# Performance work log

Hardware: AMD Instinct MI355X
Metric: run time of the kernel (lower is better)

The kernel has to match this reference:

```python
import jax, jax.numpy as jnp
import numpy as np

# Complete binary tree: B trees, L leaves each, processed level-synchronously.
B, L, IN_DIM, MEM = 64, 1024, 300, 256


def setup_inputs() -> dict:
    key = jax.random.key(0)
    ks = jax.random.split(key, 6)
    s = 0.05
    embs = jax.random.normal(ks[0], (B, L, IN_DIM), dtype=jnp.float32)
    # Leaf module: c = cx(x); h = sigmoid(ox(x)) * tanh(c)
    Wcx = jax.random.normal(ks[1], (MEM, IN_DIM), dtype=jnp.float32) * s
    bcx = jnp.zeros((MEM,), jnp.float32)
    Wox = jax.random.normal(ks[2], (MEM, IN_DIM), dtype=jnp.float32) * s
    box = jnp.zeros((MEM,), jnp.float32)
    # Composer: 4 gates (i, lf, rf, u), each gate = Linear(lh) + Linear(rh).
    # Stacked: Wl/Wr have shape [4, MEM, MEM]; biases [4, MEM].
    Wl = jax.random.normal(ks[3], (4, MEM, MEM), dtype=jnp.float32) * s
    bl = jnp.zeros((4, MEM), jnp.float32)
    Wr = jax.random.normal(ks[4], (4, MEM, MEM), dtype=jnp.float32) * s
    br = jnp.zeros((4, MEM), jnp.float32)
    return dict(embs=embs, Wcx=Wcx, bcx=bcx, Wox=Wox, box=box,
                Wl=Wl, bl=bl, Wr=Wr, br=br)


def reference(embs, Wcx, bcx, Wox, box, Wl, bl, Wr, br):
    # Leaf module (BinaryTreeLeafModule.forward), vectorized over all leaves.
    c = jnp.einsum('blx,mx->blm', embs, Wcx) + bcx          # [B, L, MEM]
    o = jax.nn.sigmoid(jnp.einsum('blx,mx->blm', embs, Wox) + box)
    h = o * jnp.tanh(c)

    bias = bl + br                                          # [4, MEM]
    n = c.shape[1]
    while n > 1:  # log2(L) levels, static unrolled loop
        lc, rc = c[:, 0::2], c[:, 1::2]                     # [B, n/2, MEM]
        lh, rh = h[:, 0::2], h[:, 1::2]
        # All 4 gate pre-activations fused: [B, n/2, 4, MEM]
        g = (jnp.einsum('bnm,gom->bngo', lh, Wl)
             + jnp.einsum('bnm,gom->bngo', rh, Wr) + bias)
        i = jax.nn.sigmoid(g[..., 0, :])
        lf = jax.nn.sigmoid(g[..., 1, :])
        rf = jax.nn.sigmoid(g[..., 2, :])
        u = jnp.tanh(g[..., 3, :])
        c = i * u + lf * lc + rf * rc                       # composer cell
        h = jnp.tanh(c)                                     # gate_output=False path
        n //= 2

    # Root state (tree.state = (c, h)); stacked as [2, B, MEM]
    return jnp.stack([c[:, 0], h[:, 0]])
```

## Files before the change

kernel.cpp:

```cpp
#include <hip/hip_runtime.h>
#include <hip/hip_bf16.h>


typedef __attribute__((ext_vector_type(8))) short bf16x8;
typedef __attribute__((ext_vector_type(4))) float f32x4;

__device__ __forceinline__ float fsig(float x)  { return 1.f / (1.f + __expf(-x)); }
__device__ __forceinline__ float ftanh(float x) { return 1.f - 2.f / (__expf(2.f * x) + 1.f); }
__device__ __forceinline__ ushort f2bf(float x) {
    __hip_bfloat16 b = __float2bfloat16(x);
    return *reinterpret_cast<ushort*>(&b);
}

__device__ __forceinline__ void gld_lds16(const void* g, void* l) {
    __builtin_amdgcn_global_load_lds((const __attribute__((address_space(1))) void*)g,
                                     (__attribute__((address_space(3))) void*)l, 16, 0, 0);
}

__global__ void prep(const float* __restrict__ Wl,  const float* __restrict__ Wr,
                     const float* __restrict__ bl,  const float* __restrict__ br,
                     const float* __restrict__ Wcx, const float* __restrict__ Wox,
                     const float* __restrict__ bcx, const float* __restrict__ box,
                     const float* __restrict__ embs,
                     ushort* __restrict__ Wb2, ushort* __restrict__ WbL,
                     float* __restrict__ bp2, float* __restrict__ bpL,
                     ushort* __restrict__ embsB)
{
    const int gid = blockIdx.x * 256 + threadIdx.x;
    for (int i = gid; i < 524288; i += 262144) {
        int e = i & 7, slot = (i >> 3) & 3, o = (i >> 5) & 255;
        int g = (i >> 13) & 3, t = i >> 15;
        int q = slot ^ ((o >> 1) & 3);
        int k = t * 32 + q * 8 + e;
        float v = (k < 256) ? Wl[(g * 256 + o) * 256 + k]
                            : Wr[(g * 256 + o) * 256 + (k - 256)];
        Wb2[i] = f2bf(v);
    }
    if (gid < 163840) {
        int e = gid & 7, slot = (gid >> 3) & 3, o = (gid >> 5) & 255;
        int g = (gid >> 13) & 1, t = gid >> 14;
        int q = slot ^ ((o >> 1) & 3);
        int k = t * 32 + q * 8 + e;
        float v = 0.f;
        if (k < 300) v = g ? Wox[o * 300 + k] : Wcx[o * 300 + k];
        WbL[gid] = f2bf(v);
    }
    if (gid < 1024) bp2[gid] = bl[gid] + br[gid];
    if (gid < 512) {
        int g = gid >> 8, o = gid & 255;
        bpL[gid] = g ? box[o] : bcx[o];
    }
    for (int i = gid; i < 65536 * 80; i += 262144) {
        int row = i / 80;
        int k = (i - row * 80) * 4;
        float4 v = make_float4(0.f, 0.f, 0.f, 0.f);
        if (k < 300) v = *(const float4*)(embs + (size_t)row * 300 + k);
        ushort4 o4;
        o4.x = f2bf(v.x); o4.y = f2bf(v.y); o4.z = f2bf(v.z); o4.w = f2bf(v.w);
        *(ushort4*)(embsB + (size_t)row * 320 + k) = o4;
    }
}

template<int NG, int HALVES, int MODE>
__global__ __launch_bounds__(256, 4)
void mfma_gemm(const ushort* __restrict__ A,
               const ushort* __restrict__ Wb,
               const float* __restrict__ bp,
               const float* __restrict__ Cprev,
               float* __restrict__ c_out,
               ushort* __restrict__ h_out,
               int M)
{
    constexpr int K = HALVES * 32;
    constexpr int OW = 128 / NG;
    __shared__ __align__(16) ushort As[2][512 * 8];
    __shared__ __align__(16) ushort Bs[2][512 * 8];

    const int tid = threadIdx.x;
    const int wid = tid >> 6, ln = tid & 63;
    const int lq = ln >> 4, lr = ln & 15;
    const int wm = wid >> 1, wn = wid & 1;
    const int rowBlk = blockIdx.x * 128;
    const int o0 = blockIdx.y * OW;

    f32x4 acc[4][4];
#pragma unroll
    for (int m = 0; m < 4; ++m)
#pragma unroll
        for (int f = 0; f < 4; ++f) acc[m][f] = f32x4{0.f, 0.f, 0.f, 0.f};

    const int ar0 = tid >> 2,  as0 = tid & 3;
    const int ar1 = ar0 + 64;
    const int aq0 = (as0 - ((ar0 >> 1) & 3)) & 3;
    const int aq1 = (as0 - ((ar1 >> 1) & 3)) & 3;
    const ushort* aP0 = A + (size_t)min(rowBlk + ar0, M - 1) * K + aq0 * 8;
    const ushort* aP1 = A + (size_t)min(rowBlk + ar1, M - 1) * K + aq1 * 8;
    const int bj0 = tid >> 2,        bs0 = tid & 3;
    const int bj1 = (tid + 256) >> 2;
    const int bg0 = bj0 / OW, bo0 = o0 + (bj0 & (OW - 1));
    const int bg1 = bj1 / OW, bo1 = o0 + (bj1 & (OW - 1));
    const ushort* bP0 = Wb + ((size_t)bg0 * 1024 + bo0 * 4 + bs0) * 8;
    const ushort* bP1 = Wb + ((size_t)bg1 * 1024 + bo1 * 4 + bs0) * 8;
    constexpr size_t BSTR = (size_t)NG * 1024 * 8;

    const int aSw = (lq + ((lr >> 1) & 3)) & 3;
    const int bSw = lq ^ ((lr >> 1) & 3);
    int aOff[4];
#pragma unroll
    for (int m = 0; m < 4; ++m)
        aOff[m] = ((wm * 64 + m * 16 + lr) * 4 + aSw) * 8;
    int bOff[4];
#pragma unroll
    for (int f = 0; f < 4; ++f)
        bOff[f] = ((f * 32 + wn * 16 + lr) * 4 + bSw) * 8;

    gld_lds16(aP0, &As[0][tid * 8]);
    gld_lds16(aP1, &As[0][(tid + 256) * 8]);
    gld_lds16(bP0, &Bs[0][tid * 8]);
    gld_lds16(bP1, &Bs[0][(tid + 256) * 8]);

#pragma unroll
    for (int h = 0; h < HALVES; ++h) {
        __syncthreads();
        const int cur = h & 1;
        if (h + 1 < HALVES) {
            gld_lds16(aP0 + (size_t)(h + 1) * 32, &As[cur ^ 1][tid * 8]);
            gld_lds16(aP1 + (size_t)(h + 1) * 32, &As[cur ^ 1][(tid + 256) * 8]);
            gld_lds16(bP0 + (size_t)(h + 1) * BSTR, &Bs[cur ^ 1][tid * 8]);
            gld_lds16(bP1 + (size_t)(h + 1) * BSTR, &Bs[cur ^ 1][(tid + 256) * 8]);
        }
        bf16x8 a[4];
#pragma unroll
        for (int m = 0; m < 4; ++m)
            a[m] = *(const bf16x8*)&As[cur][aOff[m]];
#pragma unroll
        for (int f = 0; f < 4; ++f) {
            bf16x8 b = *(const bf16x8*)&Bs[cur][bOff[f]];
#pragma unroll
            for (int m = 0; m < 4; ++m)
                acc[m][f] = __builtin_amdgcn_mfma_f32_16x16x32_bf16(a[m], b, acc[m][f], 0, 0, 0);
        }
    }

#pragma unroll
    for (int m = 0; m < 4; ++m) {
        const int row0 = rowBlk + wm * 64 + m * 16 + lq * 4;
        if constexpr (MODE == 0) {
#pragma unroll
            for (int ob = 0; ob < 2; ++ob) {
                const int col = o0 + ob * 32 + wn * 16 + lr;
                const float bc = bp[col], bo = bp[256 + col];
#pragma unroll
                for (int j = 0; j < 4; ++j) {
                    int row = row0 + j;
                    if (row < M) {
                        float cv = acc[m][ob][j] + bc;
                        float ov = acc[m][2 + ob][j] + bo;
                        c_out[(size_t)row * 256 + col] = cv;
                        h_out[(size_t)row * 256 + col] = f2bf(fsig(ov) * ftanh(cv));
                    }
                }
            }
        } else {
            const int col = o0 + wn * 16 + lr;
            const float bi  = bp[col],       blf = bp[256 + col];
            const float brf = bp[512 + col], bu  = bp[768 + col];
#pragma unroll
            for (int j = 0; j < 4; ++j) {
                int row = row0 + j;
                if (row < M) {
                    float gi = fsig(acc[m][0][j] + bi);
                    float lf = fsig(acc[m][1][j] + blf);
                    float rf = fsig(acc[m][2][j] + brf);
                    float gu = ftanh(acc[m][3][j] + bu);
                    float lc = Cprev[(size_t)row * 512 + col];
                    float rc = Cprev[(size_t)row * 512 + 256 + col];
                    float cv = gi * gu + lf * lc + rf * rc;
                    c_out[(size_t)row * 256 + col] = cv;
                    h_out[(size_t)row * 256 + col] = f2bf(ftanh(cv));
                }
            }
        }
    }
}


__global__ __launch_bounds__(512, 1)
void tail_lstm(const ushort* __restrict__ hin,
               const float* __restrict__ cin,
               const ushort* __restrict__ Wb,
               const float* __restrict__ bp,
               float* __restrict__ dout)
{
    __shared__ __align__(16) ushort H0[32 * 256];
    __shared__ __align__(16) ushort H1[16 * 256];
    __shared__ __align__(16) float  C0[32 * 256];
    __shared__ __align__(16) float  C1[16 * 256];

    const int b = blockIdx.x;
    const int tid = threadIdx.x;
    const int wid = tid >> 6, ln = tid & 63;
    const int lq = ln >> 4, lr = ln & 15;

    for (int ct = tid; ct < 1024; ct += 512) {
        int pr = ct >> 5, pc = ct & 31;
        bf16x8 v = *(const bf16x8*)(hin + ((size_t)(b * 32 + pr) * 256 + pc * 8));
        *(bf16x8*)&H0[pr * 256 + ((pc ^ ((pr >> 1) & 7)) * 8)] = v;
    }
    for (int i = tid; i < 2048; i += 512)
        *(float4*)&C0[i * 4] = *(const float4*)(cin + (size_t)b * 32 * 256 + i * 4);
    __syncthreads();

    int o_[2], sl_[2];
    const ushort* bB[2];
#pragma unroll
    for (int of = 0; of < 2; ++of) {
        o_[of] = wid * 32 + of * 16 + lr;
        sl_[of] = lq ^ ((o_[of] >> 1) & 3);
        bB[of] = Wb + (size_t)(o_[of] * 4 + sl_[of]) * 8;
    }
    const float bi  = bp[o_[0]],       blf = bp[256 + o_[0]];
    const float brf = bp[512 + o_[0]], bu  = bp[768 + o_[0]];
    const float bi1  = bp[o_[1]],       blf1 = bp[256 + o_[1]];
    const float brf1 = bp[512 + o_[1]], bu1  = bp[768 + o_[1]];

#pragma unroll 1
    for (int lvl = 0; lvl < 5; ++lvl) {
        const int npo = 16 >> lvl;
        const ushort* Hin = (lvl & 1) ? H1 : H0;
        ushort*       Hout = (lvl & 1) ? H0 : H1;
        const float*  Cin = (lvl & 1) ? C1 : C0;
        float*        Cout = (lvl & 1) ? C0 : C1;

        f32x4 acc[2][4];
#pragma unroll
        for (int of = 0; of < 2; ++of)
#pragma unroll
            for (int g = 0; g < 4; ++g) acc[of][g] = f32x4{0.f, 0.f, 0.f, 0.f};

        bf16x8 b0[2][4], b1[2][4], a0, a1;
#pragma unroll
        for (int of = 0; of < 2; ++of)
#pragma unroll
            for (int g = 0; g < 4; ++g)
                b0[of][g] = *(const bf16x8*)(bB[of] + (size_t)g * 8192);
        {
            int pr = 2 * lr, pc = lq;
            a0 = *(const bf16x8*)&Hin[pr * 256 + ((pc ^ ((pr >> 1) & 7)) * 8)];
        }

#pragma unroll 1
        for (int ks = 0; ks < 16; ks += 2) {
            if (ks + 1 < 16) {
#pragma unroll
                for (int of = 0; of < 2; ++of)
#pragma unroll
                    for (int g = 0; g < 4; ++g)
                        b1[of][g] = *(const bf16x8*)(bB[of] + (size_t)((ks + 1) * 4 + g) * 8192);
                int pr = 2 * lr + ((ks + 1) >> 3), pc = lq + ((ks + 1) & 7) * 4;
                a1 = *(const bf16x8*)&Hin[pr * 256 + ((pc ^ ((pr >> 1) & 7)) * 8)];
            }
#pragma unroll
            for (int of = 0; of < 2; ++of)
#pragma unroll
                for (int g = 0; g < 4; ++g)
                    acc[of][g] = __builtin_amdgcn_mfma_f32_16x16x32_bf16(a0, b0[of][g], acc[of][g], 0, 0, 0);
            if (ks + 2 < 16) {
#pragma unroll
                for (int of = 0; of < 2; ++of)
#pragma unroll
                    for (int g = 0; g < 4; ++g)
                        b0[of][g] = *(const bf16x8*)(bB[of] + (size_t)((ks + 2) * 4 + g) * 8192);
                int pr = 2 * lr + ((ks + 2) >> 3), pc = lq + ((ks + 2) & 7) * 4;
                a0 = *(const bf16x8*)&Hin[pr * 256 + ((pc ^ ((pr >> 1) & 7)) * 8)];
            }
#pragma unroll
            for (int of = 0; of < 2; ++of)
#pragma unroll
                for (int g = 0; g < 4; ++g)
                    acc[of][g] = __builtin_amdgcn_mfma_f32_16x16x32_bf16(a1, b1[of][g], acc[of][g], 0, 0, 0);
        }

#pragma unroll
        for (int of = 0; of < 2; ++of) {
            const int col = o_[of];
            const float vbi  = of ? bi1 : bi,   vblf = of ? blf1 : blf;
            const float vbrf = of ? brf1 : brf, vbu  = of ? bu1 : bu;
#pragma unroll
            for (int j = 0; j < 4; ++j) {
                int row = lq * 4 + j;
                if (row < npo) {
                    float gi = fsig(acc[of][0][j] + vbi);
                    float lf = fsig(acc[of][1][j] + vblf);
                    float rf = fsig(acc[of][2][j] + vbrf);
                    float gu = ftanh(acc[of][3][j] + vbu);
                    float lc = Cin[(2 * row) * 256 + col];
                    float rc = Cin[(2 * row + 1) * 256 + col];
                    float cv = gi * gu + lf * lc + rf * rc;
                    float hv = ftanh(cv);
                    if (lvl == 4) {
                        dout[b * 256 + col] = cv;
                        dout[16384 + b * 256 + col] = hv;
                    } else {
                        Cout[row * 256 + col] = cv;
                        Hout[row * 256 + (((col >> 3) ^ ((row >> 1) & 7)) * 8) + (col & 7)] = f2bf(hv);
                    }
                }
            }
        }
        __syncthreads();
    }
}


extern "C" void kernel_launch(void* const* d_in, const int* in_sizes, int n_in,
                              void* d_out, int out_size, void* d_ws, size_t ws_size,
                              hipStream_t stream)
{
    const float* embs = (const float*)d_in[0];
    const float* Wcx  = (const float*)d_in[1];
    const float* bcx  = (const float*)d_in[2];
    const float* Wox  = (const float*)d_in[3];
    const float* box  = (const float*)d_in[4];
    const float* Wl   = (const float*)d_in[5];
    const float* bl   = (const float*)d_in[6];
    const float* Wr   = (const float*)d_in[7];
    const float* br   = (const float*)d_in[8];

    char* p = (char*)d_ws;
    ushort* Wb2 = (ushort*)p;  p += (size_t)524288 * 2;
    ushort* WbL = (ushort*)p;  p += (size_t)163840 * 2;
    float*  bp2 = (float*)p;   p += 1024 * 4;
    float*  bpL = (float*)p;   p += 512 * 4;
    float*  c0  = (float*)p;   p += (size_t)65536 * 256 * 4;
    ushort* h0  = (ushort*)p;  p += (size_t)65536 * 256 * 2;
    char* X = p;
    ushort* embsB = (ushort*)X;
    float*  cA = (float*)X;
    ushort* hA = (ushort*)(X + (size_t)32768 * 256 * 4);
    float*  cB = (float*)(X + (size_t)48 * 1024 * 1024);
    ushort* hB = (ushort*)(X + (size_t)64 * 1024 * 1024);

    prep<<<1024, 256, 0, stream>>>(Wl, Wr, bl, br, Wcx, Wox, bcx, box, embs,
                                   Wb2, WbL, bp2, bpL, embsB);

    mfma_gemm<2, 10, 0><<<dim3(512, 4), 256, 0, stream>>>(
        embsB, WbL, bpL, nullptr, c0, h0, 65536);

    mfma_gemm<4, 16, 1><<<dim3(256, 8), 256, 0, stream>>>(
        h0, Wb2, bp2, c0, cA, hA, 32768);
    mfma_gemm<4, 16, 1><<<dim3(128, 8), 256, 0, stream>>>(
        hA, Wb2, bp2, cA, cB, hB, 16384);
    mfma_gemm<4, 16, 1><<<dim3(64, 8), 256, 0, stream>>>(
        hB, Wb2, bp2, cB, cA, hA, 8192);
    mfma_gemm<4, 16, 1><<<dim3(32, 8), 256, 0, stream>>>(
        hA, Wb2, bp2, cA, cB, hB, 4096);
    mfma_gemm<4, 16, 1><<<dim3(16, 8), 256, 0, stream>>>(
        hB, Wb2, bp2, cB, cA, hA, 2048);

    tail_lstm<<<64, 512, 0, stream>>>(
        hA, cA, Wb2, bp2, (float*)d_out);
}
```

Baseline: 260.3 us.

## Triple-buffer GEMM LDS loads and fold one more level into tail kernel

The GEMM moves from a double-buffered to a triple-buffered LDS pipeline, prefetching two K-slices ahead with explicit vmcnt waits and a raw barrier, and lowers the launch-bounds occupancy hint from 4 to 3. The tail kernel now starts one level earlier (64 nodes per tree) and handles that level with a two-row-tile MFMA pass, which removes the last small GEMM launch. This trades LDS footprint and occupancy for deeper load latency hiding, and replaces a poorly occupied launch with extra serial work inside 64 blocks.

```diff
diff --git a/kernel.cpp b/kernel.cpp
--- a/kernel.cpp
+++ b/kernel.cpp
@@ -61,8 +61,9 @@
     }
 }
 
+
 template<int NG, int HALVES, int MODE>
-__global__ __launch_bounds__(256, 4)
+__global__ __launch_bounds__(256, 3)
 void mfma_gemm(const ushort* __restrict__ A,
                const ushort* __restrict__ Wb,
                const float* __restrict__ bp,
@@ -73,8 +74,8 @@
 {
     constexpr int K = HALVES * 32;
     constexpr int OW = 128 / NG;
-    __shared__ __align__(16) ushort As[2][512 * 8];
-    __shared__ __align__(16) ushort Bs[2][512 * 8];
+    __shared__ __align__(16) ushort As[3][512 * 8];
+    __shared__ __align__(16) ushort Bs[3][512 * 8];
 
     const int tid = threadIdx.x;
     const int wid = tid >> 6, ln = tid & 63;
@@ -118,27 +119,42 @@
     gld_lds16(aP1, &As[0][(tid + 256) * 8]);
     gld_lds16(bP0, &Bs[0][tid * 8]);
     gld_lds16(bP1, &Bs[0][(tid + 256) * 8]);
+    gld_lds16(aP0 + 32, &As[1][tid * 8]);
+    gld_lds16(aP1 + 32, &As[1][(tid + 256) * 8]);
+    gld_lds16(bP0 + BSTR, &Bs[1][tid * 8]);
+    gld_lds16(bP1 + BSTR, &Bs[1][(tid + 256) * 8]);
+    asm volatile("s_waitcnt vmcnt(4)" ::: "memory");
+    __builtin_amdgcn_s_barrier();
+    __builtin_amdgcn_sched_barrier(0);
 
 #pragma unroll
     for (int h = 0; h < HALVES; ++h) {
-        __syncthreads();
-        const int cur = h & 1;
-        if (h + 1 < HALVES) {
-            gld_lds16(aP0 + (size_t)(h + 1) * 32, &As[cur ^ 1][tid * 8]);
-            gld_lds16(aP1 + (size_t)(h + 1) * 32, &As[cur ^ 1][(tid + 256) * 8]);
-            gld_lds16(bP0 + (size_t)(h + 1) * BSTR, &Bs[cur ^ 1][tid * 8]);
-            gld_lds16(bP1 + (size_t)(h + 1) * BSTR, &Bs[cur ^ 1][(tid + 256) * 8]);
+        const ushort* Ac = &As[h % 3][0];
+        const ushort* Bc = &Bs[h % 3][0];
+        if (h + 2 < HALVES) {
+            ushort* An = &As[(h + 2) % 3][0];
+            ushort* Bn = &Bs[(h + 2) % 3][0];
+            gld_lds16(aP0 + (size_t)(h + 2) * 32, An + tid * 8);
+            gld_lds16(aP1 + (size_t)(h + 2) * 32, An + (tid + 256) * 8);
+            gld_lds16(bP0 + (size_t)(h + 2) * BSTR, Bn + tid * 8);
+            gld_lds16(bP1 + (size_t)(h + 2) * BSTR, Bn + (tid + 256) * 8);
         }
         bf16x8 a[4];
 #pragma unroll
         for (int m = 0; m < 4; ++m)
-            a[m] = *(const bf16x8*)&As[cur][aOff[m]];
+            a[m] = *(const bf16x8*)(Ac + aOff[m]);
 #pragma unroll
         for (int f = 0; f < 4; ++f) {
-            bf16x8 b = *(const bf16x8*)&Bs[cur][bOff[f]];
+            bf16x8 b = *(const bf16x8*)(Bc + bOff[f]);
 #pragma unroll
             for (int m = 0; m < 4; ++m)
                 acc[m][f] = __builtin_amdgcn_mfma_f32_16x16x32_bf16(a[m], b, acc[m][f], 0, 0, 0);
+        }
+        if (h + 1 < HALVES) {
+            if (h + 2 < HALVES) asm volatile("s_waitcnt vmcnt(4)" ::: "memory");
+            else                asm volatile("s_waitcnt vmcnt(0)" ::: "memory");
+            __builtin_amdgcn_s_barrier();
+            __builtin_amdgcn_sched_barrier(0);
         }
     }
 
@@ -192,23 +208,23 @@
                const float* __restrict__ bp,
                float* __restrict__ dout)
 {
-    __shared__ __align__(16) ushort H0[32 * 256];
-    __shared__ __align__(16) ushort H1[16 * 256];
-    __shared__ __align__(16) float  C0[32 * 256];
-    __shared__ __align__(16) float  C1[16 * 256];
+    __shared__ __align__(16) ushort H0[64 * 256];
+    __shared__ __align__(16) ushort H1[32 * 256];
+    __shared__ __align__(16) float  C0[64 * 256];
+    __shared__ __align__(16) float  C1[32 * 256];
 
     const int b = blockIdx.x;
     const int tid = threadIdx.x;
     const int wid = tid >> 6, ln = tid & 63;
     const int lq = ln >> 4, lr = ln & 15;
 
-    for (int ct = tid; ct < 1024; ct += 512) {
+    for (int ct = tid; ct < 2048; ct += 512) {
         int pr = ct >> 5, pc = ct & 31;
-        bf16x8 v = *(const bf16x8*)(hin + ((size_t)(b * 32 + pr) * 256 + pc * 8));
+        bf16x8 v = *(const bf16x8*)(hin + ((size_t)(b * 64 + pr) * 256 + pc * 8));
         *(bf16x8*)&H0[pr * 256 + ((pc ^ ((pr >> 1) & 7)) * 8)] = v;
     }
-    for (int i = tid; i < 2048; i += 512)
-        *(float4*)&C0[i * 4] = *(const float4*)(cin + (size_t)b * 32 * 256 + i * 4);
+    for (int i = tid; i < 4096; i += 512)
+        *(float4*)&C0[i * 4] = *(const float4*)(cin + (size_t)b * 64 * 256 + i * 4);
     __syncthreads();
 
     int o_[2], sl_[2];
@@ -219,14 +235,102 @@
         sl_[of] = lq ^ ((o_[of] >> 1) & 3);
         bB[of] = Wb + (size_t)(o_[of] * 4 + sl_[of]) * 8;
     }
-    const float bi  = bp[o_[0]],       blf = bp[256 + o_[0]];
-    const float brf = bp[512 + o_[0]], bu  = bp[768 + o_[0]];
+    const float bi0  = bp[o_[0]],       blf0 = bp[256 + o_[0]];
+    const float brf0 = bp[512 + o_[0]], bu0  = bp[768 + o_[0]];
     const float bi1  = bp[o_[1]],       blf1 = bp[256 + o_[1]];
     const float brf1 = bp[512 + o_[1]], bu1  = bp[768 + o_[1]];
 
+    {
+        f32x4 acc[2][2][4];
+#pragma unroll
+        for (int m = 0; m < 2; ++m)
+#pragma unroll
+            for (int of = 0; of < 2; ++of)
+#pragma unroll
+                for (int g = 0; g < 4; ++g) acc[m][of][g] = f32x4{0.f, 0.f, 0.f, 0.f};
+
+        bf16x8 b0[2][4], b1[2][4], a0[2], a1[2];
+#pragma unroll
+        for (int of = 0; of < 2; ++of)
+#pragma unroll
+            for (int g = 0; g < 4; ++g)
+                b0[of][g] = *(const bf16x8*)(bB[of] + (size_t)g * 8192);
+#pragma unroll
+        for (int m = 0; m < 2; ++m) {
+            int pr = 32 * m + 2 * lr, pc = lq;
+            a0[m] = *(const bf16x8*)&H0[pr * 256 + ((pc ^ ((pr >> 1) & 7)) * 8)];
+        }
+
 #pragma unroll 1
-    for (int lvl = 0; lvl < 5; ++lvl) {
-        const int npo = 16 >> lvl;
+        for (int ks = 0; ks < 16; ks += 2) {
+            if (ks + 1 < 16) {
+#pragma unroll
+                for (int of = 0; of < 2; ++of)
+#pragma unroll
+                    for (int g = 0; g < 4; ++g)
+                        b1[of][g] = *(const bf16x8*)(bB[of] + (size_t)((ks + 1) * 4 + g) * 8192);
+#pragma unroll
+                for (int m = 0; m < 2; ++m) {
+                    int pr = 32 * m + 2 * lr + ((ks + 1) >> 3), pc = lq + ((ks + 1) & 7) * 4;
+                    a1[m] = *(const bf16x8*)&H0[pr * 256 + ((pc ^ ((pr >> 1) & 7)) * 8)];
+                }
+            }
+#pragma unroll
+            for (int m = 0; m < 2; ++m)
+#pragma unroll
+                for (int of = 0; of < 2; ++of)
+#pragma unroll
+                    for (int g = 0; g < 4; ++g)
+                        acc[m][of][g] = __builtin_amdgcn_mfma_f32_16x16x32_bf16(a0[m], b0[of][g], acc[m][of][g], 0, 0, 0);
+            if (ks + 2 < 16) {
+#pragma unroll
+                for (int of = 0; of < 2; ++of)
+#pragma unroll
+                    for (int g = 0; g < 4; ++g)
+                        b0[of][g] = *(const bf16x8*)(bB[of] + (size_t)((ks + 2) * 4 + g) * 8192);
+#pragma unroll
+                for (int m = 0; m < 2; ++m) {
+                    int pr = 32 * m + 2 * lr + ((ks + 2) >> 3), pc = lq + ((ks + 2) & 7) * 4;
+                    a0[m] = *(const bf16x8*)&H0[pr * 256 + ((pc ^ ((pr >> 1) & 7)) * 8)];
+                }
+            }
+#pragma unroll
+            for (int m = 0; m < 2; ++m)
+#pragma unroll
+                for (int of = 0; of < 2; ++of)
+#pragma unroll
+                    for (int g = 0; g < 4; ++g)
+                        acc[m][of][g] = __builtin_amdgcn_mfma_f32_16x16x32_bf16(a1[m], b1[of][g], acc[m][of][g], 0, 0, 0);
+        }
+
+#pragma unroll
+        for (int m = 0; m < 2; ++m)
+#pragma unroll
+        for (int of = 0; of < 2; ++of) {
+            const int col = o_[of];
+            const float vbi  = of ? bi1 : bi0,   vblf = of ? blf1 : blf0;
+            const float vbrf = of ? brf1 : brf0, vbu  = of ? bu1 : bu0;
+#pragma unroll
+            for (int j = 0; j < 4; ++j) {
+                int row = m * 16 + lq * 4 + j;
+                float gi = fsig(acc[m][of][0][j] + vbi);
+                float lf = fsig(acc[m][of][1][j] + vblf);
+                float rf = fsig(acc[m][of][2][j] + vbrf);
+                float gu = ftanh(acc[m][of][3][j] + vbu);
+                float lc = C0[(2 * row) * 256 + col];
+                float rc = C0[(2 * row + 1) * 256 + col];
+                float cv = gi * gu + lf * lc + rf * rc;
+                float hv = ftanh(cv);
+                C1[row * 256 + col] = cv;
+                H1[row * 256 + (((col >> 3) ^ ((row >> 1) & 7)) * 8) + (col & 7)] = f2bf(hv);
+            }
+        }
+        __syncthreads();
+    }
+
+#pragma unroll 1
+    for (int lvl = 1; lvl < 6; ++lvl) {
+        const int npo = 32 >> lvl;
         const ushort* Hin = (lvl & 1) ? H1 : H0;
         ushort*       Hout = (lvl & 1) ? H0 : H1;
         const float*  Cin = (lvl & 1) ? C1 : C0;
@@ -284,8 +388,8 @@
 #pragma unroll
         for (int of = 0; of < 2; ++of) {
             const int col = o_[of];
-            const float vbi  = of ? bi1 : bi,   vblf = of ? blf1 : blf;
-            const float vbrf = of ? brf1 : brf, vbu  = of ? bu1 : bu;
+            const float vbi  = of ? bi1 : bi0,   vblf = of ? blf1 : blf0;
+            const float vbrf = of ? brf1 : brf0, vbu  = of ? bu1 : bu0;
 #pragma unroll
             for (int j = 0; j < 4; ++j) {
                 int row = lq * 4 + j;
@@ -298,7 +402,7 @@
                     float rc = Cin[(2 * row + 1) * 256 + col];
                     float cv = gi * gu + lf * lc + rf * rc;
                     float hv = ftanh(cv);
-                    if (lvl == 4) {
+                    if (lvl == 5) {
                         dout[b * 256 + col] = cv;
                         dout[16384 + b * 256 + col] = hv;
                     } else {
@@ -355,9 +459,7 @@
         hB, Wb2, bp2, cB, cA, hA, 8192);
     mfma_gemm<4, 16, 1><<<dim3(32, 8), 256, 0, stream>>>(
         hA, Wb2, bp2, cA, cB, hB, 4096);
-    mfma_gemm<4, 16, 1><<<dim3(16, 8), 256, 0, stream>>>(
-        hB, Wb2, bp2, cB, cA, hA, 2048);
 
     tail_lstm<<<64, 512, 0, stream>>>(
-        hA, cA, Wb2, bp2, (float*)d_out);
-}
+        hB, cB, Wb2, bp2, (float*)d_out);
+}
```

Result: slower. 270.4 us (+3.9%).
